# Optimization experiments

Measured on AMD Instinct MI355X. Metric: run time of the kernel, lower is better.

The kernel has to match this reference:

```python
import jax, jax.numpy as jnp
import numpy as np

N, C, T, VQ, VK = 8, 64, 256, 90, 50
S, L = 4, 4  # num_subset, lag_len
EPS = 1e-5


def conv1x1(x, W, b):
    # x: [n, c_in, t, v], W: [c_out, c_in], b: [c_out]
    return jnp.einsum('oc,nctv->notv', W, x) + b[None, :, None, None]


def batchnorm(x, gamma, beta):
    # training-mode BatchNorm2d with batch statistics (biased variance)
    m = jnp.mean(x, axis=(0, 2, 3), keepdims=True)
    v = jnp.mean((x - m) ** 2, axis=(0, 2, 3), keepdims=True)
    xn = (x - m) * jax.lax.rsqrt(v + EPS)
    return xn * gamma[None, :, None, None] + beta[None, :, None, None]


def setup_inputs() -> dict:
    key = jax.random.key(0)
    ks = jax.random.split(key, 20)
    f = lambda k, shp: jax.random.normal(k, shp, dtype=jnp.float32)
    w = 0.05
    return {
        'x_q': f(ks[0], (N, C, T, VQ)),
        'x_k': f(ks[1], (N, C, T, VK)),
        'x_v': f(ks[2], (N, C, T, VK)),
        'Wq': f(ks[3], (S * C, C)) * w, 'bq': f(ks[4], (S * C,)) * w,
        'Wk': f(ks[5], (S * C, C)) * w, 'bk': f(ks[6], (S * C,)) * w,
        'Wv': f(ks[7], (C, C)) * w, 'bv': f(ks[8], (C,)) * w,
        'Wout': f(ks[9], (C, S * C)) * w, 'bout': f(ks[10], (C,)) * w,
        'gamma_out': jnp.ones((C,), jnp.float32), 'beta_out': jnp.zeros((C,), jnp.float32),
        'Wdown': f(ks[11], (C, C)) * w, 'bdown': f(ks[12], (C,)) * w,
        'gamma_down': jnp.ones((C,), jnp.float32), 'beta_down': jnp.zeros((C,), jnp.float32),
    }


def reference(x_q, x_k, x_v, Wq, bq, Wk, bk, Wv, bv, Wout, bout,
              gamma_out, beta_out, Wdown, bdown, gamma_down, beta_down):
    Tq = T - L
    # query projection on truncated window -> [n, s, c, Tq, VQ]
    q = conv1x1(x_q[:, :, :Tq, :], Wq, bq).reshape(N, S, C, Tq, VQ)
    # 1x1 conv commutes with time slicing: project keys once over full T
    k_full = conv1x1(x_k, Wk, bk).reshape(N, S, C, T, VK)
    scale = (C * Tq) ** 0.5
    # multi-lag scores, each [n, s, VQ, VK]
    atts = [jnp.einsum('nsctu,nsctv->nsuv', q, k_full[:, :, :, l:Tq + l, :]) / scale
            for l in range(L + 1)]
    stack = jnp.stack(atts)  # [L+1, n, s, VQ, VK]
    p_att = (jnp.max(stack, axis=0) + jnp.mean(stack, axis=0)) * 0.5
    att = jax.nn.softmax(p_att, axis=-1)  # dropout = identity (eval)
    v = conv1x1(x_v, Wv, bv)  # [n, c, T, VK]
    y = jnp.einsum('nsvu,nctu->nsctv', att, v)  # [n, s, c, T, VQ]
    y = y.reshape(N, S * C, T, VQ)
    y = batchnorm(conv1x1(y, Wout, bout), gamma_out, beta_out)
    d = batchnorm(conv1x1(x_q, Wdown, bdown), gamma_down, beta_down)
    return jax.nn.leaky_relu(d + y, 0.1)
```

## Files before the change

### kernel.cpp

```cpp
#include <hip/hip_runtime.h>
#include <hip/hip_bf16.h>

typedef __hip_bfloat16 bf16;
typedef __attribute__((ext_vector_type(8))) short short8;
typedef __attribute__((ext_vector_type(16))) float f32x16;

__device__ __forceinline__ float b2f(bf16 x) { return __bfloat162float(x); }
__device__ __forceinline__ bf16  f2b(float x) { return __float2bfloat16(x); }
__device__ __forceinline__ short f2bs(float x) {
    bf16 h = __float2bfloat16(x);
    return *reinterpret_cast<short*>(&h);
}
__device__ __forceinline__ float s2f(short s) {
    bf16 h; *reinterpret_cast<short*>(&h) = s; return __bfloat162float(h);
}
__device__ __forceinline__ void gload_lds16(const void* g, void* l) {
    __builtin_amdgcn_global_load_lds(
        (const __attribute__((address_space(1))) void*)g,
        (__attribute__((address_space(3))) void*)l, 16, 0, 0);
}

constexpr int N_ = 8, C_ = 64, T_ = 256, VQ_ = 90, VK_ = 50, S_ = 4, L_ = 4;
constexpr int Tq_ = T_ - L_;
constexpr int NL  = L_ + 1;
constexpr int COLS = T_ * VQ_;
constexpr float EPSf = 1e-5f;
constexpr int NSL = 16;

union SMemG {
    struct { short A[8 * 256 * 8]; short B[8 * 128 * 8]; } ab;
    short buf[4][64 * 66];
};

__global__ __launch_bounds__(64)
void k0_precompute(const float* __restrict__ Wq, const float* __restrict__ bq,
                   const float* __restrict__ Wk, const float* __restrict__ bk,
                   short* __restrict__ MtA, float* __restrict__ bMp,
                   float* __restrict__ wb, float* __restrict__ cb) {
    int s  = blockIdx.x >> 6;
    int ci = blockIdx.x & 63;
    int cj = threadIdx.x;
    float m = 0.f;
    for (int c = 0; c < C_; ++c)
        m += Wq[(s * C_ + c) * C_ + ci] * Wk[(s * C_ + c) * C_ + cj];
    MtA[((cj >> 3) * 256 + s * C_ + ci) * 8 + (cj & 7)] = f2bs(m);
    if (cj == 0) {
        float v = 0.f;
        for (int c = 0; c < C_; ++c)
            v += Wq[(s * C_ + c) * C_ + ci] * bk[s * C_ + c];
        bMp[s * C_ + ci] = v;
    }
    if (ci == 0) {
        float v = 0.f;
        for (int c = 0; c < C_; ++c)
            v += bq[s * C_ + c] * Wk[(s * C_ + c) * C_ + cj];
        wb[s * C_ + cj] = v;
        if (cj == 0) {
            float v2 = 0.f;
            for (int c = 0; c < C_; ++c)
                v2 += bq[s * C_ + c] * bk[s * C_ + c];
            cb[s] = v2;
        }
    }
}

__global__ __launch_bounds__(256)
void k0b_wos(const float* __restrict__ Wout, const float* __restrict__ bout,
             const float* __restrict__ Wv, const float* __restrict__ bv,
             short* __restrict__ WosA, float* __restrict__ bos) {
    int cj = blockIdx.x;
    __shared__ float wvcol[C_];
    if (threadIdx.x < C_) wvcol[threadIdx.x] = Wv[threadIdx.x * C_ + cj];
    __syncthreads();
    int p = threadIdx.x;
    int s = p >> 6, o = p & 63;
    float acc = 0.f;
    for (int c = 0; c < C_; ++c)
        acc += Wout[o * (S_ * C_) + s * C_ + c] * wvcol[c];
    WosA[((cj >> 3) * 256 + p) * 8 + (cj & 7)] = f2bs(acc);
    if (cj == 0 && p < C_) {
        float a = bout[p];
        for (int k = 0; k < S_ * C_; ++k)
            a += Wout[p * (S_ * C_) + k] * bv[k & 63];
        bos[p] = a;
    }
}

__global__ __launch_bounds__(256)
void k0c_xqt(const float* __restrict__ xq, short* __restrict__ xqT) {
    int tt = blockIdx.x;
    int g  = blockIdx.y;
    int n  = blockIdx.z;
    int t0 = tt * 4;
    __shared__ float lds[8 * 360];
    int tid = threadIdx.x;
    const float* src = xq + ((size_t)(n * 64 + g * 8) * 256 + t0) * 90;
#pragma unroll
    for (int i = tid; i < 720; i += 256) {
        int c = i / 90, r = i % 90;
        float4 v = *(const float4*)(src + (size_t)c * 23040 + r * 4);
        *(float4*)(&lds[c * 360 + r * 4]) = v;
    }
    __syncthreads();
    for (int e = tid; e < 4 * 96; e += 256) {
        int t = e / 96, u = e % 96;
        short8 pk;
#pragma unroll
        for (int j = 0; j < 8; ++j)
            pk[j] = (u < 90) ? f2bs(lds[j * 360 + t * 90 + u]) : (short)0;
        *(short8*)(xqT + (((size_t)(n * 8 + g) * 256 + t0 + t) * 96 + u) * 8) = pk;
    }
}

__global__ __launch_bounds__(256)
void k1_mfma(const float* __restrict__ x_k, const short* __restrict__ MtA,
             const float* __restrict__ bMp, short* __restrict__ kqT) {
    int tb = blockIdx.x, n = blockIdx.y;
    int t0 = tb * 2;
    __shared__ SMemG u;
    __shared__ float bmp_s[256];
    __shared__ float xs[3200];
    int tid = threadIdx.x;
    if (tid < 256) bmp_s[tid] = bMp[tid];
    for (int i = tid; i < 2048; i += 256)
        ((short8*)u.ab.A)[i] = ((const short8*)MtA)[i];
#pragma unroll
    for (int p = 0; p < 2; ++p) {
        for (int i4 = tid; i4 < 800; i4 += 256) {
            int c32 = i4 / 25, o = i4 % 25;
            *(float4*)(&xs[c32 * 100 + o * 4]) =
                *(const float4*)(x_k + ((size_t)(n * 64 + p * 32 + c32) * 256 + t0) * 50 + o * 4);
        }
        __syncthreads();
        for (int m = tid; m < 512; m += 256) {
            int kgl = m >> 7, c = m & 127, t = c >> 6, v = c & 63;
            short8 pk;
            if (v < VK_) {
#pragma unroll
                for (int j = 0; j < 8; ++j) pk[j] = f2bs(xs[(kgl * 8 + j) * 100 + t * 50 + v]);
            } else {
#pragma unroll
                for (int j = 0; j < 8; ++j) pk[j] = 0;
            }
            *(short8*)(u.ab.B + ((p * 4 + kgl) * 128 + c) * 8) = pk;
        }
        __syncthreads();
    }
    int wave = tid >> 6, lane = tid & 63, q = lane >> 5, c32 = lane & 31;
    f32x16 acc[2][4];
#pragma unroll
    for (int mt = 0; mt < 2; ++mt) {
#pragma unroll
        for (int r = 0; r < 16; ++r) {
            float b = bmp_s[wave * 64 + mt * 32 + (r & 3) + 8 * (r >> 2) + 4 * q];
#pragma unroll
            for (int nt = 0; nt < 4; ++nt) acc[mt][nt][r] = b;
        }
    }
#pragma unroll
    for (int ks = 0; ks < 4; ++ks) {
        int kg = 2 * ks + q;
        short8 a0 = *(const short8*)(u.ab.A + (kg * 256 + wave * 64 + c32) * 8);
        short8 a1 = *(const short8*)(u.ab.A + (kg * 256 + wave * 64 + 32 + c32) * 8);
#pragma unroll
        for (int nt = 0; nt < 4; ++nt) {
            short8 b = *(const short8*)(u.ab.B + (kg * 128 + nt * 32 + c32) * 8);
            acc[0][nt] = __builtin_amdgcn_mfma_f32_32x32x16_bf16(a0, b, acc[0][nt], 0, 0, 0);
            acc[1][nt] = __builtin_amdgcn_mfma_f32_32x32x16_bf16(a1, b, acc[1][nt], 0, 0, 0);
        }
    }
    __syncthreads();
    int ns = n * 4 + wave;
    for (int t = 0; t < 2; ++t) {
#pragma unroll
        for (int mt = 0; mt < 2; ++mt)
#pragma unroll
            for (int ntl = 0; ntl < 2; ++ntl) {
                f32x16 A = acc[mt][t * 2 + ntl];
                int cloc = ntl * 32 + c32;
#pragma unroll
                for (int r = 0; r < 16; ++r) {
                    int ci = mt * 32 + (r & 3) + 8 * (r >> 2) + 4 * q;
                    u.buf[wave][cloc * 66 + ci] = f2bs(A[r]);
                }
            }
        __syncthreads();
        if (lane < VK_) {
#pragma unroll
            for (int g = 0; g < 8; ++g) {
                short8 pk;
#pragma unroll
                for (int j = 0; j < 8; ++j) pk[j] = u.buf[wave][lane * 66 + g * 8 + j];
                *(short8*)(kqT + ((((size_t)ns * 8 + g) * 256 + t0 + t) * VK_ + lane) * 8) = pk;
            }
        }
        __syncthreads();
    }
}

__global__ __launch_bounds__(128)
void k3b_kbsum(const float* __restrict__ x_k, const float* __restrict__ wb,
               const float* __restrict__ cb, float* __restrict__ kbsum) {
    int cjg = blockIdx.x;
    int n = blockIdx.y;
    __shared__ float S[2][NL][VK_];
    for (int pr = threadIdx.x; pr < 2 * VK_; pr += 128) {
        int cjl = pr / VK_, v = pr % VK_;
        const float* base = x_k + ((size_t)(n * 64 + cjg * 2 + cjl) * 256) * VK_ + v;
        float a = 0.f;
        for (int t = 0; t < Tq_; ++t) a += base[t * VK_];
        S[cjl][0][v] = a;
        float run = a;
        for (int l = 1; l < NL; ++l) {
            run += base[(251 + l) * VK_] - base[(l - 1) * VK_];
            S[cjl][l][v] = run;
        }
    }
    __syncthreads();
    for (int e = threadIdx.x; e < S_ * NL * VK_; e += 128) {
        int s = e / (NL * VK_), r = e % (NL * VK_), l = r / VK_, v = r % VK_;
        float a = wb[s * 64 + cjg * 2] * S[0][l][v] + wb[s * 64 + cjg * 2 + 1] * S[1][l][v];
        if (cjg == 0) a += (float)Tq_ * cb[s];
        atomicAdd(&kbsum[((size_t)(n * 4 + s) * NL + l) * VK_ + v], a);
    }
}

__global__ __launch_bounds__(256)
void k3_mfma(const short* __restrict__ xqT, const short* __restrict__ kqT,
             float* __restrict__ partial) {
    int lin = blockIdx.x + 16 * blockIdx.y;
    int grp = lin & 7;
    int idx = lin >> 3;
    int slice = grp + 8 * (idx >> 3);
    int sub = idx & 7;
    int n = slice >> 3, g = slice & 7;
    int s = sub >> 1, half = sub & 1;
    int ns = n * 4 + s;
    int gx = g * 2 + half;
    __shared__ __align__(16) short sbuf[2][15872];
    int tid = threadIdx.x;
    int wave = tid >> 6, lane = tid & 63;
    int q = lane >> 5, nl = lane & 31;
    int n1 = wave * 64 + nl, n2 = n1 + 32;
    int nc1 = min(n1, 249), nc2 = min(n2, 249);
    int l1 = nc1 / VK_, v1 = nc1 % VK_;
    int l2 = nc2 / VK_, v2 = nc2 % VK_;
    int bo1 = ((q + l1) * VK_ + v1) * 8;
    int bo2 = ((q + l2) * VK_ + v2) * 8;
    int ao = (q * 96 + nl) * 8;
    f32x16 acc[6];
#pragma unroll
    for (int i = 0; i < 6; ++i)
#pragma unroll
        for (int r = 0; r < 16; ++r) acc[i][r] = 0.f;
    const short* asrc = xqT + (size_t)(n * 8 + g) * 256 * 768;
    const short* bsrc = kqT + (size_t)(ns * 8 + g) * 256 * 400;
    int c0 = half * 10, nch = half ? 11 : 10;
    int ncall = (wave == 3) ? 7 : 8;

    auto stage = [&](int buf, int ch) {
        int t0 = ch * 12;
        const short8* aS = (const short8*)(asrc + t0 * 768);
        const short8* bS = (const short8*)(bsrc + t0 * 400);
        char* db = (char*)(&sbuf[buf][0]);
        for (int it = 0; it < ncall; ++it) {
            int call = wave * 8 + it;
            int i = call * 64 + lane;
            const void* gsrc = (i < 1152) ? (const void*)(aS + i)
                                          : (const void*)(bS + min(i - 1152, 799));
            gload_lds16(gsrc, db + call * 1024);
        }
    };

    stage(0, c0);
    for (int ci = 0; ci < nch; ++ci) {
        int cur = ci & 1;
        if (ci + 1 < nch) {
            stage(cur ^ 1, c0 + ci + 1);
            if (wave == 3) asm volatile("s_waitcnt vmcnt(7)" ::: "memory");
            else           asm volatile("s_waitcnt vmcnt(8)" ::: "memory");
        } else {
            asm volatile("s_waitcnt vmcnt(0)" ::: "memory");
        }
        __builtin_amdgcn_s_barrier();
        const short* xa  = &sbuf[cur][0];
        const short* kbs = &sbuf[cur][9216];
        __builtin_amdgcn_s_setprio(1);
#pragma unroll
        for (int ts = 0; ts < 6; ++ts) {
            short8 a0 = *(const short8*)(xa + ao + ts * 1536);
            short8 a1 = *(const short8*)(xa + ao + 256 + ts * 1536);
            short8 a2 = *(const short8*)(xa + ao + 512 + ts * 1536);
            short8 b0 = *(const short8*)(kbs + bo1 + ts * 800);
            short8 b1 = *(const short8*)(kbs + bo2 + ts * 800);
            acc[0] = __builtin_amdgcn_mfma_f32_32x32x16_bf16(a0, b0, acc[0], 0, 0, 0);
            acc[1] = __builtin_amdgcn_mfma_f32_32x32x16_bf16(a1, b0, acc[1], 0, 0, 0);
            acc[2] = __builtin_amdgcn_mfma_f32_32x32x16_bf16(a2, b0, acc[2], 0, 0, 0);
            acc[3] = __builtin_amdgcn_mfma_f32_32x32x16_bf16(a0, b1, acc[3], 0, 0, 0);
            acc[4] = __builtin_amdgcn_mfma_f32_32x32x16_bf16(a1, b1, acc[4], 0, 0, 0);
            acc[5] = __builtin_amdgcn_mfma_f32_32x32x16_bf16(a2, b1, acc[5], 0, 0, 0);
        }
        __builtin_amdgcn_s_setprio(0);
        __builtin_amdgcn_s_barrier();
    }
#pragma unroll
    for (int inb = 0; inb < 2; ++inb) {
        int ng = wave * 64 + inb * 32 + nl;
        if (ng < 250) {
            int l = ng / VK_, v = ng % VK_;
            float* pb = partial + ((((size_t)ns * 5 + l) * 90) * NSL + gx) * VK_ + v;
#pragma unroll
            for (int iu = 0; iu < 3; ++iu) {
#pragma unroll
                for (int r = 0; r < 16; ++r) {
                    int u2 = iu * 32 + (r & 3) + 8 * (r >> 2) + 4 * q;
                    if (u2 < 90) pb[(size_t)u2 * NSL * VK_] = acc[inb * 3 + iu][r];
                }
            }
        }
    }
}

__global__ __launch_bounds__(256)
void k4_softmax(const float* __restrict__ partial, const float* __restrict__ kbsum,
                bf16* __restrict__ att) {
    int ug = blockIdx.x;
    int ns = blockIdx.y;
    int u0 = ug * 15;
    __shared__ float sred[NL * 15 * VK_];
    for (int idx = threadIdx.x; idx < NL * 15 * VK_; idx += 256) {
        int l = idx / (15 * VK_), r = idx % (15 * VK_);
        int u2 = r / VK_, v = r % VK_;
        const float* p = partial + (((size_t)(ns * NL + l) * 90 + u0 + u2) * NSL) * VK_ + v;
        float a = 0.f;
#pragma unroll
        for (int sl = 0; sl < NSL; ++sl) a += p[sl * VK_];
        sred[idx] = a;
    }
    __syncthreads();
    if (threadIdx.x < 15) {
        int u2 = threadIdx.x;
        const float inv_scale = rsqrtf((float)(C_ * Tq_));
        float pv[VK_];
        float pmax = -1e30f;
#pragma unroll
        for (int v = 0; v < VK_; ++v) {
            float mx = -1e30f, mn = 0.f;
#pragma unroll
            for (int l = 0; l < NL; ++l) {
                float sl = (sred[(l * 15 + u2) * VK_ + v] + kbsum[((size_t)ns * NL + l) * VK_ + v]) * inv_scale;
                mx = fmaxf(mx, sl); mn += sl;
            }
            pv[v] = 0.5f * (mx + mn * (1.f / NL));
            pmax = fmaxf(pmax, pv[v]);
        }
        float sum = 0.f;
#pragma unroll
        for (int v = 0; v < VK_; ++v) { pv[v] = __expf(pv[v] - pmax); sum += pv[v]; }
        float inv = 1.f / sum;
#pragma unroll
        for (int v = 0; v < VK_; ++v)
            att[((size_t)ns * VQ_ + u0 + u2) * VK_ + v] = f2b(pv[v] * inv);
    }
}

__global__ __launch_bounds__(256)
void k5_mfma(const float* __restrict__ x_v, const short* __restrict__ WosA,
             short* __restrict__ wv_pack) {
    int tb = blockIdx.x, n = blockIdx.y;
    int t0 = tb * 2;
    __shared__ SMemG u;
    __shared__ float xs[3200];
    int tid = threadIdx.x;
    for (int i = tid; i < 2048; i += 256)
        ((short8*)u.ab.A)[i] = ((const short8*)WosA)[i];
#pragma unroll
    for (int p = 0; p < 2; ++p) {
        for (int i4 = tid; i4 < 800; i4 += 256) {
            int c32 = i4 / 25, o = i4 % 25;
            *(float4*)(&xs[c32 * 100 + o * 4]) =
                *(const float4*)(x_v + ((size_t)(n * 64 + p * 32 + c32) * 256 + t0) * 50 + o * 4);
        }
        __syncthreads();
        for (int m = tid; m < 512; m += 256) {
            int kgl = m >> 7, c = m & 127, t = c >> 6, v = c & 63;
            short8 pk;
            if (v < VK_) {
#pragma unroll
                for (int j = 0; j < 8; ++j) pk[j] = f2bs(xs[(kgl * 8 + j) * 100 + t * 50 + v]);
            } else {
#pragma unroll
                for (int j = 0; j < 8; ++j) pk[j] = 0;
            }
            *(short8*)(u.ab.B + ((p * 4 + kgl) * 128 + c) * 8) = pk;
        }
        __syncthreads();
    }
    int wave = tid >> 6, lane = tid & 63, q = lane >> 5, c32 = lane & 31;
    f32x16 acc[2][4];
#pragma unroll
    for (int mt = 0; mt < 2; ++mt)
#pragma unroll
        for (int nt = 0; nt < 4; ++nt)
#pragma unroll
            for (int r = 0; r < 16; ++r) acc[mt][nt][r] = 0.f;
#pragma unroll
    for (int ks = 0; ks < 4; ++ks) {
        int kg = 2 * ks + q;
        short8 a0 = *(const short8*)(u.ab.A + (kg * 256 + wave * 64 + c32) * 8);
        short8 a1 = *(const short8*)(u.ab.A + (kg * 256 + wave * 64 + 32 + c32) * 8);
#pragma unroll
        for (int nt = 0; nt < 4; ++nt) {
            short8 b = *(const short8*)(u.ab.B + (kg * 128 + nt * 32 + c32) * 8);
            acc[0][nt] = __builtin_amdgcn_mfma_f32_32x32x16_bf16(a0, b, acc[0][nt], 0, 0, 0);
            acc[1][nt] = __builtin_amdgcn_mfma_f32_32x32x16_bf16(a1, b, acc[1][nt], 0, 0, 0);
        }
    }
    __syncthreads();
    for (int t = 0; t < 2; ++t) {
#pragma unroll
        for (int mt = 0; mt < 2; ++mt)
#pragma unroll
            for (int ntl = 0; ntl < 2; ++ntl) {
                f32x16 A = acc[mt][t * 2 + ntl];
                int cloc = ntl * 32 + c32;
#pragma unroll
                for (int r = 0; r < 16; ++r) {
                    int o = mt * 32 + (r & 3) + 8 * (r >> 2) + 4 * q;
                    u.buf[wave][cloc * 66 + o] = f2bs(A[r]);
                }
            }
        __syncthreads();
        short* dst = wv_pack + (((size_t)(n * 256 + t0 + t)) * 32 + wave * 8) * 512;
#pragma unroll
        for (int vg = 0; vg < 8; ++vg) {
            short8 pk;
#pragma unroll
            for (int j = 0; j < 8; ++j) pk[j] = u.buf[wave][(vg * 8 + j) * 66 + lane];
            *(short8*)(dst + (size_t)vg * 512 + lane * 8) = pk;
        }
        __syncthreads();
    }
}

__global__ __launch_bounds__(256)
void k6_mfma(const bf16* __restrict__ att, const short* __restrict__ wv_pack,
             const float* __restrict__ bos, bf16* __restrict__ out_pre) {
    int tc = blockIdx.x, n = blockIdx.y;
    __shared__ __align__(16) short att_p[32 * 96 * 8];
    __shared__ float bos_s[64];
    int tid = threadIdx.x;
    if (tid < 64) bos_s[tid] = bos[tid];
    for (int m = tid; m < 96 * 256; m += 256) {
        int u2 = m >> 8, k = m & 255;
        int s = k >> 6, vs = k & 63;
        short val = 0;
        if (u2 < 90 && vs < VK_) {
            bf16 h = att[((size_t)(n * 4 + s) * 90 + u2) * VK_ + vs];
            val = *reinterpret_cast<short*>(&h);
        }
        att_p[((k >> 3) * 96 + u2) * 8 + (k & 7)] = val;
    }
    __syncthreads();
    int wave = tid >> 6, lane = tid & 63;
    int q = lane >> 5, c = lane & 31;
    int t = tc * 4 + wave;
    f32x16 acc[6];
#pragma unroll
    for (int ot = 0; ot < 2; ++ot)
#pragma unroll
        for (int r = 0; r < 16; ++r) {
            float b = bos_s[ot * 32 + (r & 3) + 8 * (r >> 2) + 4 * q];
            acc[ot * 3 + 0][r] = b; acc[ot * 3 + 1][r] = b; acc[ot * 3 + 2][r] = b;
        }
    const short* wbase = wv_pack + (size_t)(n * 256 + t) * (32 * 512);
#pragma unroll
    for (int st = 0; st < 16; ++st) {
        int gq = 2 * st + q;
        short8 a0 = *(const short8*)(wbase + (gq * 64 + c) * 8);
        short8 a1 = *(const short8*)(wbase + (gq * 64 + 32 + c) * 8);
        short8 b0 = *(const short8*)(att_p + (gq * 96 + c) * 8);
        short8 b1 = *(const short8*)(att_p + (gq * 96 + 32 + c) * 8);
        short8 b2 = *(const short8*)(att_p + (gq * 96 + 64 + c) * 8);
        acc[0] = __builtin_amdgcn_mfma_f32_32x32x16_bf16(a0, b0, acc[0], 0, 0, 0);
        acc[1] = __builtin_amdgcn_mfma_f32_32x32x16_bf16(a0, b1, acc[1], 0, 0, 0);
        acc[2] = __builtin_amdgcn_mfma_f32_32x32x16_bf16(a0, b2, acc[2], 0, 0, 0);
        acc[3] = __builtin_amdgcn_mfma_f32_32x32x16_bf16(a1, b0, acc[3], 0, 0, 0);
        acc[4] = __builtin_amdgcn_mfma_f32_32x32x16_bf16(a1, b1, acc[4], 0, 0, 0);
        acc[5] = __builtin_amdgcn_mfma_f32_32x32x16_bf16(a1, b2, acc[5], 0, 0, 0);
    }
#pragma unroll
    for (int ot = 0; ot < 2; ++ot)
#pragma unroll
        for (int ut = 0; ut < 3; ++ut) {
            int u2 = ut * 32 + c;
            if (u2 < 90) {
                f32x16 A = acc[ot * 3 + ut];
#pragma unroll
                for (int r = 0; r < 16; ++r) {
                    int o = ot * 32 + (r & 3) + 8 * (r >> 2) + 4 * q;
                    out_pre[((size_t)(n * 64 + o) * 256 + t) * 90 + u2] = f2b(A[r]);
                }
            }
        }
}

__global__ __launch_bounds__(256)
void k7_mfma(const float* __restrict__ X, const float* __restrict__ W,
             const float* __restrict__ bias, bf16* __restrict__ out) {
    int cb = blockIdx.x, n = blockIdx.y;
    int col0 = cb * 256;
    __shared__ __align__(16) short A[8 * 64 * 8];
    __shared__ __align__(16) short B[8 * 256 * 8];
    __shared__ float bias_s[64];
    __shared__ float xs[2048];
    int tid = threadIdx.x;
    if (tid < 64) bias_s[tid] = bias[tid];
    for (int idx = tid; idx < 4096; idx += 256) {
        int o = idx >> 6, k = idx & 63;
        A[((k >> 3) * 64 + o) * 8 + (k & 7)] = f2bs(W[o * 64 + k]);
    }
#pragma unroll
    for (int p = 0; p < 8; ++p) {
        for (int i4 = tid; i4 < 512; i4 += 256) {
            int cl = i4 >> 6, o = i4 & 63;
            *(float4*)(&xs[cl * 256 + o * 4]) =
                *(const float4*)(X + (size_t)(n * 64 + p * 8 + cl) * COLS + col0 + o * 4);
        }
        __syncthreads();
        {
            short8 pk;
#pragma unroll
            for (int j = 0; j < 8; ++j) pk[j] = f2bs(xs[j * 256 + tid]);
            *(short8*)(B + (p * 256 + tid) * 8) = pk;
        }
        __syncthreads();
    }
    int wave = tid >> 6, lane = tid & 63, q = lane >> 5, c32 = lane & 31;
    f32x16 acc[2][2];
#pragma unroll
    for (int mt = 0; mt < 2; ++mt)
#pragma unroll
        for (int r = 0; r < 16; ++r) {
            float b = bias_s[mt * 32 + (r & 3) + 8 * (r >> 2) + 4 * q];
            acc[mt][0][r] = b; acc[mt][1][r] = b;
        }
#pragma unroll
    for (int ks = 0; ks < 4; ++ks) {
        int kg = 2 * ks + q;
        short8 a0 = *(const short8*)(A + (kg * 64 + c32) * 8);
        short8 a1 = *(const short8*)(A + (kg * 64 + 32 + c32) * 8);
#pragma unroll
        for (int i = 0; i < 2; ++i) {
            short8 b = *(const short8*)(B + (kg * 256 + (wave * 2 + i) * 32 + c32) * 8);
            acc[0][i] = __builtin_amdgcn_mfma_f32_32x32x16_bf16(a0, b, acc[0][i], 0, 0, 0);
            acc[1][i] = __builtin_amdgcn_mfma_f32_32x32x16_bf16(a1, b, acc[1][i], 0, 0, 0);
        }
    }
#pragma unroll
    for (int mt = 0; mt < 2; ++mt)
#pragma unroll
        for (int i = 0; i < 2; ++i) {
            int col = col0 + (wave * 2 + i) * 32 + c32;
#pragma unroll
            for (int r = 0; r < 16; ++r) {
                int o = mt * 32 + (r & 3) + 8 * (r >> 2) + 4 * q;
                out[(size_t)(n * 64 + o) * COLS + col] = f2b(acc[mt][i][r]);
            }
        }
}

__global__ __launch_bounds__(256)
void k8_stats(const bf16* __restrict__ out_pre, const bf16* __restrict__ d_pre,
              float* __restrict__ stats) {
    int path = blockIdx.x >> 9;
    int b = blockIdx.x & 511;
    int o = b >> 3, n = b & 7;
    const bf16* p = (path ? d_pre : out_pre) + ((size_t)n * C_ + o) * COLS;
    float s = 0.f, sq = 0.f;
    for (int i8 = threadIdx.x; i8 < COLS / 8; i8 += 256) {
        short8 v8 = *(const short8*)(p + i8 * 8);
#pragma unroll
        for (int j = 0; j < 8; ++j) {
            float x = s2f(v8[j]);
            s += x; sq += x * x;
        }
    }
#pragma unroll
    for (int off = 32; off > 0; off >>= 1) {
        s  += __shfl_down(s, off, 64);
        sq += __shfl_down(sq, off, 64);
    }
    __shared__ float red[8];
    int wid = threadIdx.x >> 6, lane = threadIdx.x & 63;
    if (lane == 0) { red[wid * 2] = s; red[wid * 2 + 1] = sq; }
    __syncthreads();
    if (threadIdx.x == 0) {
        float S = 0.f, Q = 0.f;
        for (int w2 = 0; w2 < 4; ++w2) { S += red[w2 * 2]; Q += red[w2 * 2 + 1]; }
        atomicAdd(&stats[path * 128 + o * 2], S);
        atomicAdd(&stats[path * 128 + o * 2 + 1], Q);
    }
}

__global__ __launch_bounds__(256)
void k9_final(const bf16* __restrict__ out_pre, const bf16* __restrict__ d_pre,
              const float* __restrict__ stats,
              const float* __restrict__ gamma_out, const float* __restrict__ beta_out,
              const float* __restrict__ gamma_down, const float* __restrict__ beta_down,
              float* __restrict__ out) {
    const float invM = 1.f / ((float)N_ * COLS);
    size_t total8 = (size_t)N_ * C_ * COLS / 8;
    size_t stride = (size_t)gridDim.x * blockDim.x;
    for (size_t i8 = (size_t)blockIdx.x * blockDim.x + threadIdx.x; i8 < total8; i8 += stride) {
        size_t idx = i8 * 8;
        int o = (int)((idx / COLS) % C_);
        float my = stats[o * 2] * invM;
        float vy = stats[o * 2 + 1] * invM - my * my;
        float md = stats[128 + o * 2] * invM;
        float vd = stats[128 + o * 2 + 1] * invM - md * md;
        float ay = rsqrtf(vy + EPSf) * gamma_out[o];
        float by = beta_out[o] - my * ay;
        float ad = rsqrtf(vd + EPSf) * gamma_down[o];
        float bd = beta_down[o] - md * ad;
        short8 y8 = *(const short8*)(out_pre + idx);
        short8 d8 = *(const short8*)(d_pre + idx);
        float rr[8];
#pragma unroll
        for (int j = 0; j < 8; ++j) {
            float r = (s2f(y8[j]) * ay + by) + (s2f(d8[j]) * ad + bd);
            rr[j] = r > 0.f ? r : 0.1f * r;
        }
        *(float4*)(out + idx)     = make_float4(rr[0], rr[1], rr[2], rr[3]);
        *(float4*)(out + idx + 4) = make_float4(rr[4], rr[5], rr[6], rr[7]);
    }
}

extern "C" void kernel_launch(void* const* d_in, const int* in_sizes, int n_in,
                              void* d_out, int out_size, void* d_ws, size_t ws_size,
                              hipStream_t stream) {
    (void)in_sizes; (void)n_in; (void)out_size; (void)ws_size;
    const float* x_q  = (const float*)d_in[0];
    const float* x_k  = (const float*)d_in[1];
    const float* x_v  = (const float*)d_in[2];
    const float* Wq   = (const float*)d_in[3];
    const float* bq   = (const float*)d_in[4];
    const float* Wk   = (const float*)d_in[5];
    const float* bk   = (const float*)d_in[6];
    const float* Wv   = (const float*)d_in[7];
    const float* bv   = (const float*)d_in[8];
    const float* Wout = (const float*)d_in[9];
    const float* bout = (const float*)d_in[10];
    const float* gamma_out  = (const float*)d_in[11];
    const float* beta_out   = (const float*)d_in[12];
    const float* Wdown = (const float*)d_in[13];
    const float* bdown = (const float*)d_in[14];
    const float* gamma_down = (const float*)d_in[15];
    const float* beta_down  = (const float*)d_in[16];

    char* w = (char*)d_ws;
    size_t off = 0;
    auto nxt = [&](size_t bytes) {
        char* p = w + off;
        off += (bytes + 255) & ~(size_t)255;
        return p;
    };
    short* MtA   = (short*)nxt((size_t)8 * 256 * 8 * 2);
    float* bMp   = (float*)nxt(256 * 4);
    float* wbp   = (float*)nxt((size_t)S_ * C_ * 4);
    float* cbp   = (float*)nxt((size_t)S_ * 4);
    short* WosA  = (short*)nxt((size_t)8 * 256 * 8 * 2);
    float* bos   = (float*)nxt((size_t)C_ * 4);
    float* kbsum = (float*)nxt((size_t)N_ * S_ * NL * VK_ * 4);
    bf16*  att   = (bf16*)nxt((size_t)N_ * S_ * VQ_ * VK_ * 2);
    float* stats = (float*)nxt(256 * 4);
    char* regionA = nxt((size_t)N_ * 8 * T_ * 96 * 8 * 2);
    short* xqT    = (short*)regionA;
    bf16*  out_pre = (bf16*)regionA;
    char* regionB = nxt((size_t)N_ * S_ * 8 * T_ * VK_ * 8 * 2);
    short* kqT   = (short*)regionB;
    bf16*  d_pre = (bf16*)regionB;
    char* regionC = nxt((size_t)N_ * T_ * 32 * 512 * 2);
    float* partial = (float*)regionC;
    short* wv_pack = (short*)regionC;

    hipMemsetAsync(stats, 0, 256 * 4, stream);
    hipMemsetAsync(kbsum, 0, (size_t)N_ * S_ * NL * VK_ * 4, stream);

    k0_precompute<<<S_ * C_, 64, 0, stream>>>(Wq, bq, Wk, bk, MtA, bMp, wbp, cbp);
    k0b_wos<<<C_, 256, 0, stream>>>(Wout, bout, Wv, bv, WosA, bos);
    k0c_xqt<<<dim3(64, 8, N_), 256, 0, stream>>>(x_q, xqT);
    k1_mfma<<<dim3(128, N_), 256, 0, stream>>>(x_k, MtA, bMp, kqT);
    k3b_kbsum<<<dim3(32, N_), 128, 0, stream>>>(x_k, wbp, cbp, kbsum);
    k3_mfma<<<dim3(NSL, N_ * S_), 256, 0, stream>>>(xqT, kqT, partial);
    k4_softmax<<<dim3(6, N_ * S_), 256, 0, stream>>>(partial, kbsum, att);
    k5_mfma<<<dim3(128, N_), 256, 0, stream>>>(x_v, WosA, wv_pack);
    k6_mfma<<<dim3(T_ / 4, N_), 256, 0, stream>>>(att, wv_pack, bos, out_pre);
    k7_mfma<<<dim3(COLS / 256, N_), 256, 0, stream>>>(x_q, Wdown, bdown, d_pre);
    k8_stats<<<1024, 256, 0, stream>>>(out_pre, d_pre, stats);
    k9_final<<<2880, 256, 0, stream>>>(out_pre, d_pre, stats, gamma_out, beta_out,
                                       gamma_down, beta_down, (float*)d_out);
}
```

Measured before the change: 403.3 us.

## Load weight tiles via global_load_lds and write MFMA results directly to global

Result: faster. 370.2 us (-8.2%).

```diff
diff --git a/kernel.cpp b/kernel.cpp
--- a/kernel.cpp
+++ b/kernel.cpp
@@ -2,6 +2,7 @@
 #include <hip/hip_bf16.h>
 
 typedef __hip_bfloat16 bf16;
+typedef __attribute__((ext_vector_type(4))) short short4v;
 typedef __attribute__((ext_vector_type(8))) short short8;
 typedef __attribute__((ext_vector_type(16))) float f32x16;
 
@@ -26,11 +27,6 @@
 constexpr int COLS = T_ * VQ_;
 constexpr float EPSf = 1e-5f;
 constexpr int NSL = 16;
-
-union SMemG {
-    struct { short A[8 * 256 * 8]; short B[8 * 128 * 8]; } ab;
-    short buf[4][64 * 66];
-};
 
 __global__ __launch_bounds__(64)
 void k0_precompute(const float* __restrict__ Wq, const float* __restrict__ bq,
@@ -117,19 +113,27 @@
              const float* __restrict__ bMp, short* __restrict__ kqT) {
     int tb = blockIdx.x, n = blockIdx.y;
     int t0 = tb * 2;
-    __shared__ SMemG u;
+    __shared__ __align__(16) short Ab[8 * 256 * 8];
+    __shared__ __align__(16) short Bb[8 * 128 * 8];
     __shared__ float bmp_s[256];
     __shared__ float xs[3200];
     int tid = threadIdx.x;
+    int wave = tid >> 6, lane = tid & 63, q = lane >> 5, c32 = lane & 31;
     if (tid < 256) bmp_s[tid] = bMp[tid];
-    for (int i = tid; i < 2048; i += 256)
-        ((short8*)u.ab.A)[i] = ((const short8*)MtA)[i];
+    {
+        const short8* Asrc = (const short8*)MtA;
+#pragma unroll
+        for (int it = 0; it < 8; ++it) {
+            int call = wave * 8 + it;
+            gload_lds16(Asrc + call * 64 + lane, (char*)Ab + call * 1024);
+        }
+    }
 #pragma unroll
     for (int p = 0; p < 2; ++p) {
         for (int i4 = tid; i4 < 800; i4 += 256) {
-            int c32 = i4 / 25, o = i4 % 25;
-            *(float4*)(&xs[c32 * 100 + o * 4]) =
-                *(const float4*)(x_k + ((size_t)(n * 64 + p * 32 + c32) * 256 + t0) * 50 + o * 4);
+            int cc = i4 / 25, o = i4 % 25;
+            *(float4*)(&xs[cc * 100 + o * 4]) =
+                *(const float4*)(x_k + ((size_t)(n * 64 + p * 32 + cc) * 256 + t0) * 50 + o * 4);
         }
         __syncthreads();
         for (int m = tid; m < 512; m += 256) {
@@ -142,11 +146,12 @@
 #pragma unroll
                 for (int j = 0; j < 8; ++j) pk[j] = 0;
             }
-            *(short8*)(u.ab.B + ((p * 4 + kgl) * 128 + c) * 8) = pk;
+            *(short8*)(Bb + ((p * 4 + kgl) * 128 + c) * 8) = pk;
         }
         __syncthreads();
     }
-    int wave = tid >> 6, lane = tid & 63, q = lane >> 5, c32 = lane & 31;
+    asm volatile("s_waitcnt vmcnt(0)" ::: "memory");
+    __builtin_amdgcn_s_barrier();
     f32x16 acc[2][4];
 #pragma unroll
     for (int mt = 0; mt < 2; ++mt) {
@@ -160,42 +165,32 @@
 #pragma unroll
     for (int ks = 0; ks < 4; ++ks) {
         int kg = 2 * ks + q;
-        short8 a0 = *(const short8*)(u.ab.A + (kg * 256 + wave * 64 + c32) * 8);
-        short8 a1 = *(const short8*)(u.ab.A + (kg * 256 + wave * 64 + 32 + c32) * 8);
+        short8 a0 = *(const short8*)(Ab + (kg * 256 + wave * 64 + c32) * 8);
+        short8 a1 = *(const short8*)(Ab + (kg * 256 + wave * 64 + 32 + c32) * 8);
 #pragma unroll
         for (int nt = 0; nt < 4; ++nt) {
-            short8 b = *(const short8*)(u.ab.B + (kg * 128 + nt * 32 + c32) * 8);
+            short8 b = *(const short8*)(Bb + (kg * 128 + nt * 32 + c32) * 8);
             acc[0][nt] = __builtin_amdgcn_mfma_f32_32x32x16_bf16(a0, b, acc[0][nt], 0, 0, 0);
             acc[1][nt] = __builtin_amdgcn_mfma_f32_32x32x16_bf16(a1, b, acc[1][nt], 0, 0, 0);
         }
     }
-    __syncthreads();
     int ns = n * 4 + wave;
-    for (int t = 0; t < 2; ++t) {
-#pragma unroll
-        for (int mt = 0; mt < 2; ++mt)
-#pragma unroll
-            for (int ntl = 0; ntl < 2; ++ntl) {
-                f32x16 A = acc[mt][t * 2 + ntl];
-                int cloc = ntl * 32 + c32;
-#pragma unroll
-                for (int r = 0; r < 16; ++r) {
-                    int ci = mt * 32 + (r & 3) + 8 * (r >> 2) + 4 * q;
-                    u.buf[wave][cloc * 66 + ci] = f2bs(A[r]);
+#pragma unroll
+    for (int mt = 0; mt < 2; ++mt)
+#pragma unroll
+        for (int nt = 0; nt < 4; ++nt) {
+            int t = nt >> 1, v = (nt & 1) * 32 + c32;
+            if (v < VK_) {
+                f32x16 A = acc[mt][nt];
+#pragma unroll
+                for (int rq = 0; rq < 4; ++rq) {
+                    short4v pk;
+#pragma unroll
+                    for (int rr = 0; rr < 4; ++rr) pk[rr] = f2bs(A[rq * 4 + rr]);
+                    *(short4v*)(kqT + ((((size_t)(ns * 8 + mt * 4 + rq)) * 256 + t0 + t) * VK_ + v) * 8 + 4 * q) = pk;
                 }
             }
-        __syncthreads();
-        if (lane < VK_) {
-#pragma unroll
-            for (int g = 0; g < 8; ++g) {
-                short8 pk;
-#pragma unroll
-                for (int j = 0; j < 8; ++j) pk[j] = u.buf[wave][lane * 66 + g * 8 + j];
-                *(short8*)(kqT + ((((size_t)ns * 8 + g) * 256 + t0 + t) * VK_ + lane) * 8) = pk;
-            }
-        }
-        __syncthreads();
-    }
+        }
 }
 
 __global__ __launch_bounds__(128)
@@ -369,17 +364,25 @@
              short* __restrict__ wv_pack) {
     int tb = blockIdx.x, n = blockIdx.y;
     int t0 = tb * 2;
-    __shared__ SMemG u;
+    __shared__ __align__(16) short Ab[8 * 256 * 8];
+    __shared__ __align__(16) short Bb[8 * 128 * 8];
     __shared__ float xs[3200];
     int tid = threadIdx.x;
-    for (int i = tid; i < 2048; i += 256)
-        ((short8*)u.ab.A)[i] = ((const short8*)WosA)[i];
+    int wave = tid >> 6, lane = tid & 63, q = lane >> 5, c32 = lane & 31;
+    {
+        const short8* Asrc = (const short8*)WosA;
+#pragma unroll
+        for (int it = 0; it < 8; ++it) {
+            int call = wave * 8 + it;
+            gload_lds16(Asrc + call * 64 + lane, (char*)Ab + call * 1024);
+        }
+    }
 #pragma unroll
     for (int p = 0; p < 2; ++p) {
         for (int i4 = tid; i4 < 800; i4 += 256) {
-            int c32 = i4 / 25, o = i4 % 25;
-            *(float4*)(&xs[c32 * 100 + o * 4]) =
-                *(const float4*)(x_v + ((size_t)(n * 64 + p * 32 + c32) * 256 + t0) * 50 + o * 4);
+            int cc = i4 / 25, o = i4 % 25;
+            *(float4*)(&xs[cc * 100 + o * 4]) =
+                *(const float4*)(x_v + ((size_t)(n * 64 + p * 32 + cc) * 256 + t0) * 50 + o * 4);
         }
         __syncthreads();
         for (int m = tid; m < 512; m += 256) {
@@ -392,55 +395,47 @@
 #pragma unroll
                 for (int j = 0; j < 8; ++j) pk[j] = 0;
             }
-            *(short8*)(u.ab.B + ((p * 4 + kgl) * 128 + c) * 8) = pk;
+            *(short8*)(Bb + ((p * 4 + kgl) * 128 + c) * 8) = pk;
         }
         __syncthreads();
     }
-    int wave = tid >> 6, lane = tid & 63, q = lane >> 5, c32 = lane & 31;
-    f32x16 acc[2][4];
-#pragma unroll
-    for (int mt = 0; mt < 2; ++mt)
-#pragma unroll
-        for (int nt = 0; nt < 4; ++nt)
-#pragma unroll
-            for (int r = 0; r < 16; ++r) acc[mt][nt][r] = 0.f;
+    asm volatile("s_waitcnt vmcnt(0)" ::: "memory");
+    __builtin_amdgcn_s_barrier();
+    f32x16 acc[4][2];
+#pragma unroll
+    for (int m = 0; m < 4; ++m)
+#pragma unroll
+        for (int nn2 = 0; nn2 < 2; ++nn2)
+#pragma unroll
+            for (int r = 0; r < 16; ++r) acc[m][nn2][r] = 0.f;
 #pragma unroll
     for (int ks = 0; ks < 4; ++ks) {
         int kg = 2 * ks + q;
-        short8 a0 = *(const short8*)(u.ab.A + (kg * 256 + wave * 64 + c32) * 8);
-        short8 a1 = *(const short8*)(u.ab.A + (kg * 256 + wave * 64 + 32 + c32) * 8);
-#pragma unroll
-        for (int nt = 0; nt < 4; ++nt) {
-            short8 b = *(const short8*)(u.ab.B + (kg * 128 + nt * 32 + c32) * 8);
-            acc[0][nt] = __builtin_amdgcn_mfma_f32_32x32x16_bf16(a0, b, acc[0][nt], 0, 0, 0);
-            acc[1][nt] = __builtin_amdgcn_mfma_f32_32x32x16_bf16(a1, b, acc[1][nt], 0, 0, 0);
-        }
-    }
-    __syncthreads();
-    for (int t = 0; t < 2; ++t) {
-#pragma unroll
-        for (int mt = 0; mt < 2; ++mt)
-#pragma unroll
-            for (int ntl = 0; ntl < 2; ++ntl) {
-                f32x16 A = acc[mt][t * 2 + ntl];
-                int cloc = ntl * 32 + c32;
-#pragma unroll
-                for (int r = 0; r < 16; ++r) {
-                    int o = mt * 32 + (r & 3) + 8 * (r >> 2) + 4 * q;
-                    u.buf[wave][cloc * 66 + o] = f2bs(A[r]);
-                }
-            }
-        __syncthreads();
-        short* dst = wv_pack + (((size_t)(n * 256 + t0 + t)) * 32 + wave * 8) * 512;
-#pragma unroll
-        for (int vg = 0; vg < 8; ++vg) {
-            short8 pk;
-#pragma unroll
-            for (int j = 0; j < 8; ++j) pk[j] = u.buf[wave][(vg * 8 + j) * 66 + lane];
-            *(short8*)(dst + (size_t)vg * 512 + lane * 8) = pk;
-        }
-        __syncthreads();
-    }
+        short8 bw0 = *(const short8*)(Ab + (kg * 256 + wave * 64 + c32) * 8);
+        short8 bw1 = *(const short8*)(Ab + (kg * 256 + wave * 64 + 32 + c32) * 8);
+#pragma unroll
+        for (int m = 0; m < 4; ++m) {
+            short8 ax = *(const short8*)(Bb + (kg * 128 + m * 32 + c32) * 8);
+            acc[m][0] = __builtin_amdgcn_mfma_f32_32x32x16_bf16(ax, bw0, acc[m][0], 0, 0, 0);
+            acc[m][1] = __builtin_amdgcn_mfma_f32_32x32x16_bf16(ax, bw1, acc[m][1], 0, 0, 0);
+        }
+    }
+#pragma unroll
+    for (int m = 0; m < 4; ++m)
+#pragma unroll
+        for (int nn2 = 0; nn2 < 2; ++nn2) {
+            int o = nn2 * 32 + c32;
+            int t = t0 + (m >> 1);
+            f32x16 A = acc[m][nn2];
+            size_t base = (((size_t)(n * 256 + t) * 32) + wave * 8 + (m & 1) * 4) * 512 + o * 8 + 4 * q;
+#pragma unroll
+            for (int rq = 0; rq < 4; ++rq) {
+                short4v pk;
+#pragma unroll
+                for (int rr = 0; rr < 4; ++rr) pk[rr] = f2bs(A[rq * 4 + rr]);
+                *(short4v*)(wv_pack + base + (size_t)rq * 512) = pk;
+            }
+        }
 }
 
 __global__ __launch_bounds__(256)
```
